# Performance work log

Measured on AMD Instinct MI355X. Metric: run time of the kernel, lower is better.

The kernel has to match this reference:

```python
import jax, jax.numpy as jnp
import numpy as np

N_NODES = 8192
N_EDGES = 65536
IN_DIM = 768
HIDDEN = 4096
N_CLASSES = 16


def setup_inputs() -> dict:
    key = jax.random.key(0)
    k1, k2, k3, k4 = jax.random.split(key, 4)
    x = jax.random.normal(k1, (N_NODES, IN_DIM), dtype=jnp.float32)
    edge_index = jax.random.randint(k2, (2, N_EDGES), 0, N_NODES, dtype=jnp.int64)
    # Glorot-ish init scale
    W1 = jax.random.normal(k3, (IN_DIM, HIDDEN), dtype=jnp.float32) * (1.0 / np.sqrt(IN_DIM))
    b1 = jnp.zeros((HIDDEN,), dtype=jnp.float32)
    W2 = jax.random.normal(k4, (HIDDEN, N_CLASSES), dtype=jnp.float32) * (1.0 / np.sqrt(HIDDEN))
    b2 = jnp.zeros((N_CLASSES,), dtype=jnp.float32)
    return {"x": x, "edge_index": edge_index, "W1": W1, "b1": b1, "W2": W2, "b2": b2}


def reference(x, edge_index, W1, b1, W2, b2):
    # GCNConv (PyG defaults): add self-loops, symmetric deg^-1/2 normalization,
    # transform-then-aggregate, plus bias. Then ReLU -> (dropout=identity at
    # inference) -> Linear -> log_softmax.
    N = x.shape[0]
    loops = jnp.arange(N, dtype=edge_index.dtype)
    src = jnp.concatenate([edge_index[0], loops])  # [E+N]
    dst = jnp.concatenate([edge_index[1], loops])  # [E+N]

    h = x @ W1  # [N, HIDDEN] dense GEMM

    deg = jax.ops.segment_sum(jnp.ones_like(dst, dtype=h.dtype), dst, num_segments=N)
    dinv = jnp.where(deg > 0, jax.lax.rsqrt(jnp.maximum(deg, 1e-12)), 0.0)
    norm = dinv[src] * dinv[dst]  # [E+N]

    agg = jax.ops.segment_sum(h[src] * norm[:, None], dst, num_segments=N)  # [N, HIDDEN]
    h = jax.nn.relu(agg + b1)

    logits = h @ W2 + b2  # [N, N_CLASSES]
    return jax.nn.log_softmax(logits, axis=1)
```

## Files before the change

### kernel.cpp

```cpp
#include <hip/hip_runtime.h>

#define N_NODES   8192
#define N_EDGES   65536
#define IN_DIM    768
#define HIDDEN    4096
#define N_CLASSES 16
#define SLOTS     64
#define NSLAB     16

typedef unsigned short ushort_t;
typedef __attribute__((ext_vector_type(8))) short bf16x8;
typedef __attribute__((ext_vector_type(4))) float f32x4;

__device__ __forceinline__ ushort_t f2bf(float f) {
    union { float f; unsigned i; } v; v.f = f;
    unsigned r = v.i + 0x7FFFu + ((v.i >> 16) & 1u);
    return (ushort_t)(r >> 16);
}
__device__ __forceinline__ float bf2f(ushort_t u) {
    union { unsigned i; float f; } v; v.i = ((unsigned)u) << 16; return v.f;
}

#define GLD_LDS16(gp, lp) \
    __builtin_amdgcn_global_load_lds((const __attribute__((address_space(1))) void*)(gp), \
                                     (__attribute__((address_space(3))) void*)(lp), 16, 0, 0)

__device__ __forceinline__ int esrc(const int* ei, int f32mode, int e) {
    return f32mode ? ei[e] : ei[2 * e];
}
__device__ __forceinline__ int edst(const int* ei, int f32mode, int e) {
    return f32mode ? ei[N_EDGES + e] : ei[2 * N_EDGES + 2 * e];
}

__global__ __launch_bounds__(256) void phase1(const float* __restrict__ x,
                                              ushort_t* __restrict__ xbf,
                                              const float* __restrict__ W2,
                                              ushort_t* __restrict__ W2T,
                                              const int* __restrict__ ei,
                                              int* __restrict__ cnt,
                                              int* __restrict__ slots,
                                              int* __restrict__ flag) {
    int b = blockIdx.x, t = threadIdx.x;
    if (b < 16) {
        __shared__ ushort_t ld[16 * 257];
        int k0 = b * 256;
        const float4* src = (const float4*)(W2 + (long)(k0 + t) * N_CLASSES);
        #pragma unroll
        for (int j = 0; j < 4; j++) {
            float4 v = src[j];
            ld[(j * 4 + 0) * 257 + t] = f2bf(v.x);
            ld[(j * 4 + 1) * 257 + t] = f2bf(v.y);
            ld[(j * 4 + 2) * 257 + t] = f2bf(v.z);
            ld[(j * 4 + 3) * 257 + t] = f2bf(v.w);
        }
        __syncthreads();
        #pragma unroll
        for (int c = 0; c < 16; c++)
            W2T[c * HIDDEN + k0 + t] = ld[c * 257 + t];
    } else if (b < 1552) {
        long i = (long)(b - 16) * 1024 + t;
        #pragma unroll
        for (int p = 0; p < 4; p++) {
            float4 v = ((const float4*)x)[i + p * 256];
            ushort4 r = { f2bf(v.x), f2bf(v.y), f2bf(v.z), f2bf(v.w) };
            ((ushort4*)xbf)[i + p * 256] = r;
        }
    } else {
        __shared__ int sv[256];
        int v = 0;
        for (int e = t; e < 4096; e += 256) v |= ei[2 * e + 1];
        sv[t] = v;
        __syncthreads();
        for (int off = 128; off > 0; off >>= 1) {
            if (t < off) sv[t] |= sv[t + off];
            __syncthreads();
        }
        int f = (sv[0] != 0) ? 1 : 0;
        if (b == 1552 && t == 0) *flag = f;
        int e = (b - 1552) * 256 + t;
        int s = esrc(ei, f, e), d = edst(ei, f, e);
        int p = atomicAdd(&cnt[d], 1);
        if (p < SLOTS) slots[d * SLOTS + p] = s;
    }
}

__global__ __launch_bounds__(256) void phase2(const float* __restrict__ W1,
                                              ushort_t* __restrict__ W1T,
                                              const ushort_t* __restrict__ xbf,
                                              const int* __restrict__ cnt,
                                              const int* __restrict__ slots,
                                              const int* __restrict__ ei,
                                              const int* __restrict__ flag,
                                              ushort_t* __restrict__ xagg) {
    int b = blockIdx.x, t = threadIdx.x;
    if (b < 3072) {
        __shared__ ushort_t tile[32][33];
        int n0 = (b & 127) * 32, k0 = (b >> 7) * 32;
        int tx = t & 31, ty = t >> 5;
        #pragma unroll
        for (int j = 0; j < 4; j++) {
            int k = ty * 4 + j;
            tile[k][tx] = f2bf(W1[(k0 + k) * HIDDEN + n0 + tx]);
        }
        __syncthreads();
        #pragma unroll
        for (int j = 0; j < 4; j++) {
            int n = ty * 4 + j;
            W1T[(n0 + n) * IN_DIM + k0 + tx] = tile[tx][n];
        }
        return;
    }
    if (t >= 192) return;
    int w = t >> 6, l = t & 63;
    int d = b - 3072;
    int fo = w * 256 + l * 4;
    int cd = cnt[d];
    float wd = rsqrtf((float)(cd + 1));
    ushort4 sv = *(const ushort4*)(xbf + (long)d * IN_DIM + fo);
    float a0 = wd * bf2f(sv.x), a1 = wd * bf2f(sv.y);
    float a2 = wd * bf2f(sv.z), a3 = wd * bf2f(sv.w);

    if (cd <= SLOTS) {
        const int* sl = slots + d * SLOTS;
        int j = 0;
        for (; j + 4 <= cd; j += 4) {
            int s0 = sl[j], s1 = sl[j + 1], s2 = sl[j + 2], s3 = sl[j + 3];
            float w0 = rsqrtf((float)(cnt[s0] + 1));
            float w1 = rsqrtf((float)(cnt[s1] + 1));
            float w2 = rsqrtf((float)(cnt[s2] + 1));
            float w3 = rsqrtf((float)(cnt[s3] + 1));
            ushort4 v0 = *(const ushort4*)(xbf + (long)s0 * IN_DIM + fo);
            ushort4 v1 = *(const ushort4*)(xbf + (long)s1 * IN_DIM + fo);
            ushort4 v2 = *(const ushort4*)(xbf + (long)s2 * IN_DIM + fo);
            ushort4 v3 = *(const ushort4*)(xbf + (long)s3 * IN_DIM + fo);
            a0 = fmaf(w0, bf2f(v0.x), a0); a1 = fmaf(w0, bf2f(v0.y), a1);
            a2 = fmaf(w0, bf2f(v0.z), a2); a3 = fmaf(w0, bf2f(v0.w), a3);
            a0 = fmaf(w1, bf2f(v1.x), a0); a1 = fmaf(w1, bf2f(v1.y), a1);
            a2 = fmaf(w1, bf2f(v1.z), a2); a3 = fmaf(w1, bf2f(v1.w), a3);
            a0 = fmaf(w2, bf2f(v2.x), a0); a1 = fmaf(w2, bf2f(v2.y), a1);
            a2 = fmaf(w2, bf2f(v2.z), a2); a3 = fmaf(w2, bf2f(v2.w), a3);
            a0 = fmaf(w3, bf2f(v3.x), a0); a1 = fmaf(w3, bf2f(v3.y), a1);
            a2 = fmaf(w3, bf2f(v3.z), a2); a3 = fmaf(w3, bf2f(v3.w), a3);
        }
        for (; j < cd; j++) {
            int s = sl[j];
            float ws = rsqrtf((float)(cnt[s] + 1));
            ushort4 v = *(const ushort4*)(xbf + (long)s * IN_DIM + fo);
            a0 = fmaf(ws, bf2f(v.x), a0); a1 = fmaf(ws, bf2f(v.y), a1);
            a2 = fmaf(ws, bf2f(v.z), a2); a3 = fmaf(ws, bf2f(v.w), a3);
        }
    } else {
        int f = *flag;
        for (int e = 0; e < N_EDGES; e++) {
            if (edst(ei, f, e) == d) {
                int s = esrc(ei, f, e);
                float ws = rsqrtf((float)(cnt[s] + 1));
                ushort4 v = *(const ushort4*)(xbf + (long)s * IN_DIM + fo);
                a0 = fmaf(ws, bf2f(v.x), a0); a1 = fmaf(ws, bf2f(v.y), a1);
                a2 = fmaf(ws, bf2f(v.z), a2); a3 = fmaf(ws, bf2f(v.w), a3);
            }
        }
    }
    ushort4 r = { f2bf(a0 * wd), f2bf(a1 * wd), f2bf(a2 * wd), f2bf(a3 * wd) };
    *(ushort4*)(xagg + (long)d * IN_DIM + fo) = r;
}

#define FENCE() asm volatile("" ::: "memory")
#define BAR()  do { FENCE(); __builtin_amdgcn_s_barrier(); FENCE(); } while (0)
#define VMCNT(n) asm volatile("s_waitcnt vmcnt(" #n ")" ::: "memory")
#define LGKM0()  asm volatile("s_waitcnt lgkmcnt(0)" ::: "memory")
#define PRIO(x)  __builtin_amdgcn_s_setprio(x)

__global__ __launch_bounds__(512, 2) void gemm1_fused(const ushort_t* __restrict__ A,
                                                      const ushort_t* __restrict__ Bt,
                                                      const float* __restrict__ b1,
                                                      const ushort_t* __restrict__ W2T,
                                                      float* __restrict__ part) {
    __shared__ ushort_t lds[65536];
    ushort_t* ldsA = lds;
    ushort_t* ldsB = lds + 32768;

    int t = threadIdx.x;
    int w = t >> 6, l = t & 63;
    int wm = w & 3, wn = w >> 2;
    int q = l >> 4, lm = l & 15;
    int bx = blockIdx.x & 15, by = blockIdx.x >> 4;
    int m0 = by * 256, n0 = bx * 256;

    int srow = t >> 3;
    int sg = (t & 7) ^ (srow & 7);
    const ushort_t* aS = A  + (long)(m0 + srow) * IN_DIM + sg * 8;
    const ushort_t* bS = Bt + (long)(n0 + srow) * IN_DIM + sg * 8;

#define STAGE_A(B_, h, ko) do { \
    GLD_LDS16(aS + (h) * 128 * IN_DIM + (ko),              ldsA + (B_) * 16384 + (h) * 8192 + w * 512); \
    GLD_LDS16(aS + ((h) * 128 + 64) * IN_DIM + (ko),       ldsA + (B_) * 16384 + (h) * 8192 + 4096 + w * 512); \
} while (0)
#define STAGE_B(B_, h, ko) do { \
    GLD_LDS16(bS + (h) * 128 * IN_DIM + (ko),              ldsB + (B_) * 16384 + (h) * 8192 + w * 512); \
    GLD_LDS16(bS + ((h) * 128 + 64) * IN_DIM + (ko),       ldsB + (B_) * 16384 + (h) * 8192 + 4096 + w * 512); \
} while (0)
#define LDA(dst, qm, B_) do { \
    const ushort_t* p_ = ldsA + (B_) * 16384 + (wm * 64 + (qm) * 32 + lm) * 64; \
    int x0_ = ((q) ^ (lm & 7)) * 8, x1_ = ((4 + q) ^ (lm & 7)) * 8; \
    dst[0][0] = *(const bf16x8*)(p_ + x0_);        dst[0][1] = *(const bf16x8*)(p_ + x1_); \
    dst[1][0] = *(const bf16x8*)(p_ + 1024 + x0_); dst[1][1] = *(const bf16x8*)(p_ + 1024 + x1_); \
} while (0)
#define LDB(dst, qn, B_) do { \
    const ushort_t* p_ = ldsB + (B_) * 16384 + (wn * 128 + (qn) * 64 + lm) * 64; \
    int x0_ = ((q) ^ (lm & 7)) * 8, x1_ = ((4 + q) ^ (lm & 7)) * 8; \
    dst[0][0] = *(const bf16x8*)(p_ + x0_);        dst[0][1] = *(const bf16x8*)(p_ + x1_); \
    dst[1][0] = *(const bf16x8*)(p_ + 1024 + x0_); dst[1][1] = *(const bf16x8*)(p_ + 1024 + x1_); \
    dst[2][0] = *(const bf16x8*)(p_ + 2048 + x0_); dst[2][1] = *(const bf16x8*)(p_ + 2048 + x1_); \
    dst[3][0] = *(const bf16x8*)(p_ + 3072 + x0_); dst[3][1] = *(const bf16x8*)(p_ + 3072 + x1_); \
} while (0)
#define MFMAQ(qm, qn, a_, b_) do { \
    _Pragma("unroll") for (int j_ = 0; j_ < 2; j_++) \
    _Pragma("unroll") for (int nt_ = 0; nt_ < 4; nt_++) \
    _Pragma("unroll") for (int mt_ = 0; mt_ < 2; mt_++) \
        acc[(qm) * 2 + mt_][(qn) * 4 + nt_] = __builtin_amdgcn_mfma_f32_16x16x32_bf16( \
            a_[mt_][j_], b_[nt_][j_], acc[(qm) * 2 + mt_][(qn) * 4 + nt_], 0, 0, 0); \
} while (0)

    int kA = 0, kB = 0;
    STAGE_A(0, 0, kA); STAGE_A(0, 1, kA); kA += 64;
    STAGE_B(0, 0, kB); STAGE_B(0, 1, kB); kB += 64;
    STAGE_A(1, 0, kA); STAGE_A(1, 1, kA); kA += 64;

    bf16x8 aq0[2][2], aq1[2][2], bq0[4][2], bq1[4][2];
    f32x4 acc[4][8] = {};

    VMCNT(4);
    BAR();

    #pragma unroll 1
    for (int it = 0; it < 5; ++it) {
        LDA(aq0, 0, 0); LDB(bq0, 0, 0); STAGE_B(1, 0, kB);
        BAR(); LGKM0(); PRIO(1); MFMAQ(0, 0, aq0, bq0); PRIO(0); BAR();
        LDA(aq1, 1, 0); STAGE_B(1, 1, kB); kB += 64;
        BAR(); LGKM0(); PRIO(1); MFMAQ(1, 0, aq1, bq0); PRIO(0); BAR();
        LDB(bq1, 1, 0); STAGE_A(0, 0, kA);
        BAR(); LGKM0(); PRIO(1); MFMAQ(1, 1, aq1, bq1); PRIO(0); BAR();
        STAGE_A(0, 1, kA); kA += 64;
        VMCNT(4);
        BAR(); PRIO(1); MFMAQ(0, 1, aq0, bq1); PRIO(0); BAR();
        LDA(aq0, 0, 1); LDB(bq0, 0, 1); STAGE_B(0, 0, kB);
        BAR(); LGKM0(); PRIO(1); MFMAQ(0, 0, aq0, bq0); PRIO(0); BAR();
        LDA(aq1, 1, 1); STAGE_B(0, 1, kB); kB += 64;
        BAR(); LGKM0(); PRIO(1); MFMAQ(1, 0, aq1, bq0); PRIO(0); BAR();
        LDB(bq1, 1, 1); STAGE_A(1, 0, kA);
        BAR(); LGKM0(); PRIO(1); MFMAQ(1, 1, aq1, bq1); PRIO(0); BAR();
        STAGE_A(1, 1, kA); kA += 64;
        VMCNT(4);
        BAR(); PRIO(1); MFMAQ(0, 1, aq0, bq1); PRIO(0); BAR();
    }
    LDA(aq0, 0, 0); LDB(bq0, 0, 0); STAGE_B(1, 0, kB);
    BAR(); LGKM0(); PRIO(1); MFMAQ(0, 0, aq0, bq0); PRIO(0); BAR();
    LDA(aq1, 1, 0); STAGE_B(1, 1, kB);
    BAR(); LGKM0(); PRIO(1); MFMAQ(1, 0, aq1, bq0); PRIO(0); BAR();
    LDB(bq1, 1, 0);
    BAR(); LGKM0(); PRIO(1); MFMAQ(1, 1, aq1, bq1); PRIO(0); BAR();
    VMCNT(0);
    BAR(); PRIO(1); MFMAQ(0, 1, aq0, bq1); PRIO(0); BAR();
    LDA(aq0, 0, 1); LDB(bq0, 0, 1);
    BAR(); LGKM0(); PRIO(1); MFMAQ(0, 0, aq0, bq0); PRIO(0); BAR();
    LDA(aq1, 1, 1);
    BAR(); LGKM0(); PRIO(1); MFMAQ(1, 0, aq1, bq0); PRIO(0); BAR();
    LDB(bq1, 1, 1);
    BAR(); LGKM0(); PRIO(1); MFMAQ(1, 1, aq1, bq1); PRIO(0); BAR();
    PRIO(1); MFMAQ(0, 1, aq0, bq1); PRIO(0);

    float bias[8];
    #pragma unroll
    for (int ng = 0; ng < 8; ng++) bias[ng] = b1[n0 + wn * 128 + ng * 16 + lm];
    bf16x8 w2f[2][2];
    #pragma unroll
    for (int eh = 0; eh < 2; eh++)
        #pragma unroll
        for (int kk = 0; kk < 2; kk++)
            w2f[eh][kk] = *(const bf16x8*)(W2T + (long)lm * HIDDEN + n0 + wn * 128 + eh * 64 + kk * 32 + q * 8);

    __syncthreads();
    ushort_t* slab = lds + w * 4096;
    f32x4 acc2[4] = {};
    #pragma unroll
    for (int eh = 0; eh < 2; eh++) {
        #pragma unroll
        for (int mg = 0; mg < 4; mg++)
            #pragma unroll
            for (int nt = 0; nt < 4; nt++) {
                int gc = nt * 2 + (lm >> 3);
                #pragma unroll
                for (int rr = 0; rr < 4; rr++) {
                    int row = mg * 16 + q * 4 + rr;
                    float v = acc[mg][eh * 4 + nt][rr] + bias[eh * 4 + nt];
                    v = v > 0.0f ? v : 0.0f;
                    slab[row * 64 + ((gc ^ (row & 7)) * 8) + (lm & 7)] = f2bf(v);
                }
            }
        #pragma unroll
        for (int kk = 0; kk < 2; kk++)
            #pragma unroll
            for (int mt2 = 0; mt2 < 4; mt2++) {
                bf16x8 a2 = *(const bf16x8*)(slab + (mt2 * 16 + lm) * 64 + (((kk * 4 + q) ^ (lm & 7)) * 8));
                acc2[mt2] = __builtin_amdgcn_mfma_f32_16x16x32_bf16(a2, w2f[eh][kk], acc2[mt2], 0, 0, 0);
            }
    }

    __syncthreads();
    float* psum = (float*)lds;
    if (wn == 1) {
        #pragma unroll
        for (int mt2 = 0; mt2 < 4; mt2++)
            #pragma unroll
            for (int rr = 0; rr < 4; rr++)
                psum[(wm * 64 + mt2 * 16 + q * 4 + rr) * 17 + lm] = acc2[mt2][rr];
    }
    __syncthreads();
    if (wn == 0) {
        float* pslab = part + ((long)bx * N_NODES + m0 + wm * 64) * N_CLASSES;
        #pragma unroll
        for (int mt2 = 0; mt2 < 4; mt2++)
            #pragma unroll
            for (int rr = 0; rr < 4; rr++) {
                int row = mt2 * 16 + q * 4 + rr;
                pslab[row * N_CLASSES + lm] = acc2[mt2][rr] + psum[(wm * 64 + row) * 17 + lm];
            }
    }
#undef STAGE_A
#undef STAGE_B
#undef LDA
#undef LDB
#undef MFMAQ
}

__global__ __launch_bounds__(256) void reduce_softmax(const float* __restrict__ part,
                                                      const float* __restrict__ b2,
                                                      float* __restrict__ out) {
    int t = threadIdx.x;
    int row = blockIdx.x * 16 + (t >> 4);
    int cls = t & 15;
    float v = b2[cls];
    #pragma unroll
    for (int s = 0; s < NSLAB; s++)
        v += part[((long)s * N_NODES + row) * N_CLASSES + cls];
    float mx = v;
    #pragma unroll
    for (int off = 1; off < 16; off <<= 1)
        mx = fmaxf(mx, __shfl_xor(mx, off, 64));
    float e = __expf(v - mx);
    float sm = e;
    #pragma unroll
    for (int off = 1; off < 16; off <<= 1)
        sm += __shfl_xor(sm, off, 64);
    out[(long)row * N_CLASSES + cls] = v - mx - __logf(sm);
}


extern "C" void kernel_launch(void* const* d_in, const int* in_sizes, int n_in,
                              void* d_out, int out_size, void* d_ws, size_t ws_size,
                              hipStream_t stream) {
    const float* x  = (const float*)d_in[0];
    const int*   ei = (const int*)d_in[1];
    const float* W1 = (const float*)d_in[2];
    const float* b1 = (const float*)d_in[3];
    const float* W2 = (const float*)d_in[4];
    const float* b2 = (const float*)d_in[5];
    float* out = (float*)d_out;
    char* ws = (char*)d_ws;

    float*    part  = (float*)(ws);
    ushort_t* xagg  = (ushort_t*)(ws + 16777216);
    ushort_t* xbf   = (ushort_t*)(ws + 29360128);
    ushort_t* W1T   = (ushort_t*)(ws + 41943040);
    ushort_t* W2T   = (ushort_t*)(ws + 48234496);
    int*      cnt   = (int*)(ws + 48365568);
    int*      slots = (int*)(ws + 48398336);
    int*      flag  = (int*)(ws + 50495488);

    hipMemsetAsync(cnt, 0, 32768, stream);
    phase1<<<1808, 256, 0, stream>>>(x, xbf, W2, W2T, ei, cnt, slots, flag);
    phase2<<<11264, 256, 0, stream>>>(W1, W1T, xbf, cnt, slots, ei, flag, xagg);
    gemm1_fused<<<(N_NODES / 256) * (HIDDEN / 256), 512, 0, stream>>>(xagg, W1T, b1, W2T, part);
    reduce_softmax<<<N_NODES / 16, 256, 0, stream>>>(part, b2, out);
}
```

Measured before the change: 159.7 us.

## Persistent two-tile GEMM with A reuse, move W1 transpose, repack aggregation

The fused GEMM now launches 256 blocks. Each block processes two consecutive 256-wide N tiles for one 256-row M tile and prefetches the next tile's A and B into free LDS buffers during the epilogue. The W1 transpose moves from phase2 into phase1, so the aggregation kernel only aggregates. That kernel now assigns one wavefront per node covering all 768 features, instead of three wavefronts per node with 64 idle threads per block. The aim is to cut block launch and tail overhead and to overlap the epilogue with the next tile's loads, at the cost of less GEMM parallelism (256 blocks) and more register pressure in the gather.

```diff
diff --git a/kernel.cpp b/kernel.cpp
--- a/kernel.cpp
+++ b/kernel.cpp
@@ -34,6 +34,8 @@
 
 __global__ __launch_bounds__(256) void phase1(const float* __restrict__ x,
                                               ushort_t* __restrict__ xbf,
+                                              const float* __restrict__ W1,
+                                              ushort_t* __restrict__ W1T,
                                               const float* __restrict__ W2,
                                               ushort_t* __restrict__ W2T,
                                               const int* __restrict__ ei,
@@ -65,7 +67,7 @@
             ushort4 r = { f2bf(v.x), f2bf(v.y), f2bf(v.z), f2bf(v.w) };
             ((ushort4*)xbf)[i + p * 256] = r;
         }
-    } else {
+    } else if (b < 1808) {
         __shared__ int sv[256];
         int v = 0;
         for (int e = t; e < 4096; e += 256) v |= ei[2 * e + 1];
@@ -81,45 +83,59 @@
         int s = esrc(ei, f, e), d = edst(ei, f, e);
         int p = atomicAdd(&cnt[d], 1);
         if (p < SLOTS) slots[d * SLOTS + p] = s;
+    } else {
+        __shared__ ushort_t tile[32][33];
+        int bt = b - 1808;
+        int n0 = (bt & 127) * 32, k0 = (bt >> 7) * 32;
+        int tx = t & 31, ty = t >> 5;
+        #pragma unroll
+        for (int j = 0; j < 4; j++) {
+            int k = ty * 4 + j;
+            tile[k][tx] = f2bf(W1[(k0 + k) * HIDDEN + n0 + tx]);
+        }
+        __syncthreads();
+        #pragma unroll
+        for (int j = 0; j < 4; j++) {
+            int n = ty * 4 + j;
+            W1T[(n0 + n) * IN_DIM + k0 + tx] = tile[tx][n];
+        }
     }
 }
 
-__global__ __launch_bounds__(256) void phase2(const float* __restrict__ W1,
-                                              ushort_t* __restrict__ W1T,
-                                              const ushort_t* __restrict__ xbf,
+#define ACC3(W_, v0_, v1_, v2_) do { \
+    a[0] = fmaf(W_, bf2f(v0_.x), a[0]); a[1]  = fmaf(W_, bf2f(v0_.y), a[1]); \
+    a[2] = fmaf(W_, bf2f(v0_.z), a[2]); a[3]  = fmaf(W_, bf2f(v0_.w), a[3]); \
+    a[4] = fmaf(W_, bf2f(v1_.x), a[4]); a[5]  = fmaf(W_, bf2f(v1_.y), a[5]); \
+    a[6] = fmaf(W_, bf2f(v1_.z), a[6]); a[7]  = fmaf(W_, bf2f(v1_.w), a[7]); \
+    a[8] = fmaf(W_, bf2f(v2_.x), a[8]); a[9]  = fmaf(W_, bf2f(v2_.y), a[9]); \
+    a[10] = fmaf(W_, bf2f(v2_.z), a[10]); a[11] = fmaf(W_, bf2f(v2_.w), a[11]); \
+} while (0)
+
+__global__ __launch_bounds__(256) void phase2(const ushort_t* __restrict__ xbf,
                                               const int* __restrict__ cnt,
                                               const int* __restrict__ slots,
                                               const int* __restrict__ ei,
                                               const int* __restrict__ flag,
                                               ushort_t* __restrict__ xagg) {
-    int b = blockIdx.x, t = threadIdx.x;
-    if (b < 3072) {
-        __shared__ ushort_t tile[32][33];
-        int n0 = (b & 127) * 32, k0 = (b >> 7) * 32;
-        int tx = t & 31, ty = t >> 5;
-        #pragma unroll
-        for (int j = 0; j < 4; j++) {
-            int k = ty * 4 + j;
-            tile[k][tx] = f2bf(W1[(k0 + k) * HIDDEN + n0 + tx]);
-        }
-        __syncthreads();
-        #pragma unroll
-        for (int j = 0; j < 4; j++) {
-            int n = ty * 4 + j;
-            W1T[(n0 + n) * IN_DIM + k0 + tx] = tile[tx][n];
-        }
-        return;
-    }
-    if (t >= 192) return;
+    int t = threadIdx.x;
     int w = t >> 6, l = t & 63;
-    int d = b - 3072;
-    int fo = w * 256 + l * 4;
+    int d = blockIdx.x * 4 + w;
+    int fo = l * 4;
     int cd = cnt[d];
     float wd = rsqrtf((float)(cd + 1));
-    ushort4 sv = *(const ushort4*)(xbf + (long)d * IN_DIM + fo);
-    float a0 = wd * bf2f(sv.x), a1 = wd * bf2f(sv.y);
-    float a2 = wd * bf2f(sv.z), a3 = wd * bf2f(sv.w);
-
+    float a[12];
+    {
+        const ushort_t* pr = xbf + (long)d * IN_DIM + fo;
+        ushort4 v0 = *(const ushort4*)(pr);
+        ushort4 v1 = *(const ushort4*)(pr + 256);
+        ushort4 v2 = *(const ushort4*)(pr + 512);
+        a[0] = wd * bf2f(v0.x); a[1]  = wd * bf2f(v0.y);
+        a[2] = wd * bf2f(v0.z); a[3]  = wd * bf2f(v0.w);
+        a[4] = wd * bf2f(v1.x); a[5]  = wd * bf2f(v1.y);
+        a[6] = wd * bf2f(v1.z); a[7]  = wd * bf2f(v1.w);
+        a[8] = wd * bf2f(v2.x); a[9]  = wd * bf2f(v2.y);
+        a[10] = wd * bf2f(v2.z); a[11] = wd * bf2f(v2.w);
+    }
     if (cd <= SLOTS) {
         const int* sl = slots + d * SLOTS;
         int j = 0;
@@ -129,25 +145,25 @@
             float w1 = rsqrtf((float)(cnt[s1] + 1));
             float w2 = rsqrtf((float)(cnt[s2] + 1));
             float w3 = rsqrtf((float)(cnt[s3] + 1));
-            ushort4 v0 = *(const ushort4*)(xbf + (long)s0 * IN_DIM + fo);
-            ushort4 v1 = *(const ushort4*)(xbf + (long)s1 * IN_DIM + fo);
-            ushort4 v2 = *(const ushort4*)(xbf + (long)s2 * IN_DIM + fo);
-            ushort4 v3 = *(const ushort4*)(xbf + (long)s3 * IN_DIM + fo);
-            a0 = fmaf(w0, bf2f(v0.x), a0); a1 = fmaf(w0, bf2f(v0.y), a1);
-            a2 = fmaf(w0, bf2f(v0.z), a2); a3 = fmaf(w0, bf2f(v0.w), a3);
-            a0 = fmaf(w1, bf2f(v1.x), a0); a1 = fmaf(w1, bf2f(v1.y), a1);
-            a2 = fmaf(w1, bf2f(v1.z), a2); a3 = fmaf(w1, bf2f(v1.w), a3);
-            a0 = fmaf(w2, bf2f(v2.x), a0); a1 = fmaf(w2, bf2f(v2.y), a1);
-            a2 = fmaf(w2, bf2f(v2.z), a2); a3 = fmaf(w2, bf2f(v2.w), a3);
-            a0 = fmaf(w3, bf2f(v3.x), a0); a1 = fmaf(w3, bf2f(v3.y), a1);
-            a2 = fmaf(w3, bf2f(v3.z), a2); a3 = fmaf(w3, bf2f(v3.w), a3);
+            const ushort_t* p0 = xbf + (long)s0 * IN_DIM + fo;
+            const ushort_t* p1 = xbf + (long)s1 * IN_DIM + fo;
+            const ushort_t* p2 = xbf + (long)s2 * IN_DIM + fo;
+            const ushort_t* p3 = xbf + (long)s3 * IN_DIM + fo;
+            ushort4 v00 = *(const ushort4*)(p0), v01 = *(const ushort4*)(p0 + 256), v02 = *(const ushort4*)(p0 + 512);
+            ushort4 v10 = *(const ushort4*)(p1), v11 = *(const ushort4*)(p1 + 256), v12 = *(const ushort4*)(p1 + 512);
+            ushort4 v20 = *(const ushort4*)(p2), v21 = *(const ushort4*)(p2 + 256), v22 = *(const ushort4*)(p2 + 512);
+            ushort4 v30 = *(const ushort4*)(p3), v31 = *(const ushort4*)(p3 + 256), v32 = *(const ushort4*)(p3 + 512);
+            ACC3(w0, v00, v01, v02);
+            ACC3(w1, v10, v11, v12);
+            ACC3(w2, v20, v21, v22);
+            ACC3(w3, v30, v31, v32);
         }
         for (; j < cd; j++) {
             int s = sl[j];
             float ws = rsqrtf((float)(cnt[s] + 1));
-            ushort4 v = *(const ushort4*)(xbf + (long)s * IN_DIM + fo);
-            a0 = fmaf(ws, bf2f(v.x), a0); a1 = fmaf(ws, bf2f(v.y), a1);
-            a2 = fmaf(ws, bf2f(v.z), a2); a3 = fmaf(ws, bf2f(v.w), a3);
+            const ushort_t* pp = xbf + (long)s * IN_DIM + fo;
+            ushort4 u0 = *(const ushort4*)(pp), u1 = *(const ushort4*)(pp + 256), u2 = *(const ushort4*)(pp + 512);
+            ACC3(ws, u0, u1, u2);
         }
     } else {
         int f = *flag;
@@ -155,14 +171,19 @@
             if (edst(ei, f, e) == d) {
                 int s = esrc(ei, f, e);
                 float ws = rsqrtf((float)(cnt[s] + 1));
-                ushort4 v = *(const ushort4*)(xbf + (long)s * IN_DIM + fo);
-                a0 = fmaf(ws, bf2f(v.x), a0); a1 = fmaf(ws, bf2f(v.y), a1);
-                a2 = fmaf(ws, bf2f(v.z), a2); a3 = fmaf(ws, bf2f(v.w), a3);
+                const ushort_t* pp = xbf + (long)s * IN_DIM + fo;
+                ushort4 u0 = *(const ushort4*)(pp), u1 = *(const ushort4*)(pp + 256), u2 = *(const ushort4*)(pp + 512);
+                ACC3(ws, u0, u1, u2);
             }
         }
     }
-    ushort4 r = { f2bf(a0 * wd), f2bf(a1 * wd), f2bf(a2 * wd), f2bf(a3 * wd) };
-    *(ushort4*)(xagg + (long)d * IN_DIM + fo) = r;
+    ushort_t* po = xagg + (long)d * IN_DIM + fo;
+    ushort4 r0 = { f2bf(a[0] * wd), f2bf(a[1] * wd), f2bf(a[2] * wd), f2bf(a[3] * wd) };
+    ushort4 r1 = { f2bf(a[4] * wd), f2bf(a[5] * wd), f2bf(a[6] * wd), f2bf(a[7] * wd) };
+    ushort4 r2 = { f2bf(a[8] * wd), f2bf(a[9] * wd), f2bf(a[10] * wd), f2bf(a[11] * wd) };
+    *(ushort4*)(po) = r0;
+    *(ushort4*)(po + 256) = r1;
+    *(ushort4*)(po + 512) = r2;
 }
 
 #define FENCE() asm volatile("" ::: "memory")
@@ -184,21 +205,21 @@
     int w = t >> 6, l = t & 63;
     int wm = w & 3, wn = w >> 2;
     int q = l >> 4, lm = l & 15;
-    int bx = blockIdx.x & 15, by = blockIdx.x >> 4;
-    int m0 = by * 256, n0 = bx * 256;
+    int p8 = blockIdx.x & 7, by = blockIdx.x >> 3;
+    int m0 = by * 256;
 
     int srow = t >> 3;
     int sg = (t & 7) ^ (srow & 7);
-    const ushort_t* aS = A  + (long)(m0 + srow) * IN_DIM + sg * 8;
-    const ushort_t* bS = Bt + (long)(n0 + srow) * IN_DIM + sg * 8;
+    const ushort_t* aS = A + (long)(m0 + srow) * IN_DIM + sg * 8;
+    const ushort_t* bS = Bt + (long)(p8 * 512 + srow) * IN_DIM + sg * 8;
 
 #define STAGE_A(B_, h, ko) do { \
-    GLD_LDS16(aS + (h) * 128 * IN_DIM + (ko),              ldsA + (B_) * 16384 + (h) * 8192 + w * 512); \
-    GLD_LDS16(aS + ((h) * 128 + 64) * IN_DIM + (ko),       ldsA + (B_) * 16384 + (h) * 8192 + 4096 + w * 512); \
-} while (0)
-#define STAGE_B(B_, h, ko) do { \
-    GLD_LDS16(bS + (h) * 128 * IN_DIM + (ko),              ldsB + (B_) * 16384 + (h) * 8192 + w * 512); \
-    GLD_LDS16(bS + ((h) * 128 + 64) * IN_DIM + (ko),       ldsB + (B_) * 16384 + (h) * 8192 + 4096 + w * 512); \
+    GLD_LDS16(aS + (h) * 128 * IN_DIM + (ko),            ldsA + (B_) * 16384 + (h) * 8192 + w * 512); \
+    GLD_LDS16(aS + ((h) * 128 + 64) * IN_DIM + (ko),     ldsA + (B_) * 16384 + (h) * 8192 + 4096 + w * 512); \
+} while (0)
+#define STAGE_B(bp, B_, h, ko) do { \
+    GLD_LDS16((bp) + (h) * 128 * IN_DIM + (ko),          ldsB + (B_) * 16384 + (h) * 8192 + w * 512); \
+    GLD_LDS16((bp) + ((h) * 128 + 64) * IN_DIM + (ko),   ldsB + (B_) * 16384 + (h) * 8192 + 4096 + w * 512); \
 } while (0)
 #define LDA(dst, qm, B_) do { \
     const ushort_t* p_ = ldsA + (B_) * 16384 + (wm * 64 + (qm) * 32 + lm) * 64; \
@@ -222,110 +243,124 @@
             a_[mt_][j_], b_[nt_][j_], acc[(qm) * 2 + mt_][(qn) * 4 + nt_], 0, 0, 0); \
 } while (0)
 
-    int kA = 0, kB = 0;
-    STAGE_A(0, 0, kA); STAGE_A(0, 1, kA); kA += 64;
-    STAGE_B(0, 0, kB); STAGE_B(0, 1, kB); kB += 64;
-    STAGE_A(1, 0, kA); STAGE_A(1, 1, kA); kA += 64;
+    STAGE_A(0, 0, 0); STAGE_A(0, 1, 0);
+    STAGE_B(bS, 0, 0, 0); STAGE_B(bS, 0, 1, 0);
+    STAGE_A(1, 0, 64); STAGE_A(1, 1, 64);
 
     bf16x8 aq0[2][2], aq1[2][2], bq0[4][2], bq1[4][2];
-    f32x4 acc[4][8] = {};
-
-    VMCNT(4);
-    BAR();
 
     #pragma unroll 1
-    for (int it = 0; it < 5; ++it) {
-        LDA(aq0, 0, 0); LDB(bq0, 0, 0); STAGE_B(1, 0, kB);
+    for (int tile = 0; tile < 2; ++tile) {
+        int n0 = p8 * 512 + tile * 256;
+        f32x4 acc[4][8] = {};
+        int kA = 128, kB = 64;
+
+        VMCNT(4);
+        BAR();
+
+        #pragma unroll 1
+        for (int it = 0; it < 5; ++it) {
+            LDA(aq0, 0, 0); LDB(bq0, 0, 0); STAGE_B(bS, 1, 0, kB);
+            BAR(); LGKM0(); PRIO(1); MFMAQ(0, 0, aq0, bq0); PRIO(0); BAR();
+            LDA(aq1, 1, 0); STAGE_B(bS, 1, 1, kB); kB += 64;
+            BAR(); LGKM0(); PRIO(1); MFMAQ(1, 0, aq1, bq0); PRIO(0); BAR();
+            LDB(bq1, 1, 0); STAGE_A(0, 0, kA);
+            BAR(); LGKM0(); PRIO(1); MFMAQ(1, 1, aq1, bq1); PRIO(0); BAR();
+            STAGE_A(0, 1, kA); kA += 64;
+            VMCNT(4);
+            BAR(); PRIO(1); MFMAQ(0, 1, aq0, bq1); PRIO(0); BAR();
+            LDA(aq0, 0, 1); LDB(bq0, 0, 1); STAGE_B(bS, 0, 0, kB);
+            BAR(); LGKM0(); PRIO(1); MFMAQ(0, 0, aq0, bq0); PRIO(0); BAR();
+            LDA(aq1, 1, 1); STAGE_B(bS, 0, 1, kB); kB += 64;
+            BAR(); LGKM0(); PRIO(1); MFMAQ(1, 0, aq1, bq0); PRIO(0); BAR();
+            LDB(bq1, 1, 1); STAGE_A(1, 0, kA);
+            BAR(); LGKM0(); PRIO(1); MFMAQ(1, 1, aq1, bq1); PRIO(0); BAR();
+            STAGE_A(1, 1, kA); kA += 64;
+            VMCNT(4);
+            BAR(); PRIO(1); MFMAQ(0, 1, aq0, bq1); PRIO(0); BAR();
+        }
+        LDA(aq0, 0, 0); LDB(bq0, 0, 0); STAGE_B(bS, 1, 0, kB);
         BAR(); LGKM0(); PRIO(1); MFMAQ(0, 0, aq0, bq0); PRIO(0); BAR();
-        LDA(aq1, 1, 0); STAGE_B(1, 1, kB); kB += 64;
+        LDA(aq1, 1, 0); STAGE_B(bS, 1, 1, kB);
         BAR(); LGKM0(); PRIO(1); MFMAQ(1, 0, aq1, bq0); PRIO(0); BAR();
-        LDB(bq1, 1, 0); STAGE_A(0, 0, kA);
+        LDB(bq1, 1, 0);
         BAR(); LGKM0(); PRIO(1); MFMAQ(1, 1, aq1, bq1); PRIO(0); BAR();
-        STAGE_A(0, 1, kA); kA += 64;
-        VMCNT(4);
+        VMCNT(0);
         BAR(); PRIO(1); MFMAQ(0, 1, aq0, bq1); PRIO(0); BAR();
-        LDA(aq0, 0, 1); LDB(bq0, 0, 1); STAGE_B(0, 0, kB);
+        LDA(aq0, 0, 1); LDB(bq0, 0, 1);
         BAR(); LGKM0(); PRIO(1); MFMAQ(0, 0, aq0, bq0); PRIO(0); BAR();
-        LDA(aq1, 1, 1); STAGE_B(0, 1, kB); kB += 64;
+        LDA(aq1, 1, 1);
         BAR(); LGKM0(); PRIO(1); MFMAQ(1, 0, aq1, bq0); PRIO(0); BAR();
-        LDB(bq1, 1, 1); STAGE_A(1, 0, kA);
+        LDB(bq1, 1, 1);
         BAR(); LGKM0(); PRIO(1); MFMAQ(1, 1, aq1, bq1); PRIO(0); BAR();
-        STAGE_A(1, 1, kA); kA += 64;
-        VMCNT(4);
-        BAR(); PRIO(1); MFMAQ(0, 1, aq0, bq1); PRIO(0); BAR();
-    }
-    LDA(aq0, 0, 0); LDB(bq0, 0, 0); STAGE_B(1, 0, kB);
-    BAR(); LGKM0(); PRIO(1); MFMAQ(0, 0, aq0, bq0); PRIO(0); BAR();
-    LDA(aq1, 1, 0); STAGE_B(1, 1, kB);
-    BAR(); LGKM0(); PRIO(1); MFMAQ(1, 0, aq1, bq0); PRIO(0); BAR();
-    LDB(bq1, 1, 0);
-    BAR(); LGKM0(); PRIO(1); MFMAQ(1, 1, aq1, bq1); PRIO(0); BAR();
-    VMCNT(0);
-    BAR(); PRIO(1); MFMAQ(0, 1, aq0, bq1); PRIO(0); BAR();
-    LDA(aq0, 0, 1); LDB(bq0, 0, 1);
-    BAR(); LGKM0(); PRIO(1); MFMAQ(0, 0, aq0, bq0); PRIO(0); BAR();
-    LDA(aq1, 1, 1);
-    BAR(); LGKM0(); PRIO(1); MFMAQ(1, 0, aq1, bq0); PRIO(0); BAR();
-    LDB(bq1, 1, 1);
-    BAR(); LGKM0(); PRIO(1); MFMAQ(1, 1, aq1, bq1); PRIO(0); BAR();
-    PRIO(1); MFMAQ(0, 1, aq0, bq1); PRIO(0);
-
-    float bias[8];
-    #pragma unroll
-    for (int ng = 0; ng < 8; ng++) bias[ng] = b1[n0 + wn * 128 + ng * 16 + lm];
-    bf16x8 w2f[2][2];
-    #pragma unroll
-    for (int eh = 0; eh < 2; eh++)
-        #pragma unroll
-        for (int kk = 0; kk < 2; kk++)
-            w2f[eh][kk] = *(const bf16x8*)(W2T + (long)lm * HIDDEN + n0 + wn * 128 + eh * 64 + kk * 32 + q * 8);
-
-    __syncthreads();
-    ushort_t* slab = lds + w * 4096;
-    f32x4 acc2[4] = {};
-    #pragma unroll
-    for (int eh = 0; eh < 2; eh++) {
-        #pragma unroll
-        for (int mg = 0; mg < 4; mg++)
+        PRIO(1); MFMAQ(0, 1, aq0, bq1); PRIO(0);
+
+        float bias[8];
+        #pragma unroll
+        for (int ng = 0; ng < 8; ng++) bias[ng] = b1[n0 + wn * 128 + ng * 16 + lm];
+        bf16x8 w2f[2][2];
+        #pragma unroll
+        for (int eh = 0; eh < 2; eh++)
             #pragma unroll
-            for (int nt = 0; nt < 4; nt++) {
-                int gc = nt * 2 + (lm >> 3);
+            for (int kk = 0; kk < 2; kk++)
+                w2f[eh][kk] = *(const bf16x8*)(W2T + (long)lm * HIDDEN + n0 + wn * 128 + eh * 64 + kk * 32 + q * 8);
+
+        BAR();
+        if (tile == 0) {
+            STAGE_A(0, 0, 0); STAGE_A(0, 1, 0);
+            STAGE_B(bS + 256 * IN_DIM, 0, 0, 0); STAGE_B(bS + 256 * IN_DIM, 0, 1, 0);
+        }
+        ushort_t* slab = (w < 4) ? (ldsA + 16384 + w * 4096)
+                                 : (ldsB + 16384 + (w - 4) * 4096);
+        f32x4 acc2[4] = {};
+        #pragma unroll
+        for (int eh = 0; eh < 2; eh++) {
+            #pragma unroll
+            for (int mg = 0; mg < 4; mg++)
+                #pragma unroll
+                for (int nt = 0; nt < 4; nt++) {
+                    int gc = nt * 2 + (lm >> 3);
+                    #pragma unroll
+                    for (int rr = 0; rr < 4; rr++) {
+                        int row = mg * 16 + q * 4 + rr;
+                        float v = acc[mg][eh * 4 + nt][rr] + bias[eh * 4 + nt];
+                        v = v > 0.0f ? v : 0.0f;
+                        slab[row * 64 + ((gc ^ (row & 7)) * 8) + (lm & 7)] = f2bf(v);
+                    }
+                }
+            #pragma unroll
+            for (int kk = 0; kk < 2; kk++)
+                #pragma unroll
+                for (int mt2 = 0; mt2 < 4; mt2++) {
+                    bf16x8 a2 = *(const bf16x8*)(slab + (mt2 * 16 + lm) * 64 + (((kk * 4 + q) ^ (lm & 7)) * 8));
+                    acc2[mt2] = __builtin_amdgcn_mfma_f32_16x16x32_bf16(a2, w2f[eh][kk], acc2[mt2], 0, 0, 0);
+                }
+        }
+
+        BAR();
+        if (tile == 0) { STAGE_A(1, 0, 64); STAGE_A(1, 1, 64); }
+        float* psum = (float*)(ldsB + 16384);
+        if (wn == 1) {
+            #pragma unroll
+            for (int mt2 = 0; mt2 < 4; mt2++)
+                #pragma unroll
+                for (int rr = 0; rr < 4; rr++)
+                    psum[(wm * 64 + mt2 * 16 + q * 4 + rr) * 17 + lm] = acc2[mt2][rr];
+        }
+        LGKM0();
+        BAR();
+        if (wn == 0) {
+            int bx = p8 * 2 + tile;
+            float* pslab = part + ((long)bx * N_NODES + m0 + wm * 64) * N_CLASSES;
+            #pragma unroll
+            for (int mt2 = 0; mt2 < 4; mt2++)
                 #pragma unroll
                 for (int rr = 0; rr < 4; rr++) {
-                    int row = mg * 16 + q * 4 + rr;
-                    float v = acc[mg][eh * 4 + nt][rr] + bias[eh * 4 + nt];
-                    v = v > 0.0f ? v : 0.0f;
-                    slab[row * 64 + ((gc ^ (row & 7)) * 8) + (lm & 7)] = f2bf(v);
+                    int row = mt2 * 16 + q * 4 + rr;
+                    pslab[row * N_CLASSES + lm] = acc2[mt2][rr] + psum[(wm * 64 + row) * 17 + lm];
                 }
-            }
-        #pragma unroll
-        for (int kk = 0; kk < 2; kk++)
-            #pragma unroll
-            for (int mt2 = 0; mt2 < 4; mt2++) {
-                bf16x8 a2 = *(const bf16x8*)(slab + (mt2 * 16 + lm) * 64 + (((kk * 4 + q) ^ (lm & 7)) * 8));
-                acc2[mt2] = __builtin_amdgcn_mfma_f32_16x16x32_bf16(a2, w2f[eh][kk], acc2[mt2], 0, 0, 0);
-            }
-    }
-
-    __syncthreads();
-    float* psum = (float*)lds;
-    if (wn == 1) {
-        #pragma unroll
-        for (int mt2 = 0; mt2 < 4; mt2++)
-            #pragma unroll
-            for (int rr = 0; rr < 4; rr++)
-                psum[(wm * 64 + mt2 * 16 + q * 4 + rr) * 17 + lm] = acc2[mt2][rr];
-    }
-    __syncthreads();
-    if (wn == 0) {
-        float* pslab = part + ((long)bx * N_NODES + m0 + wm * 64) * N_CLASSES;
-        #pragma unroll
-        for (int mt2 = 0; mt2 < 4; mt2++)
-            #pragma unroll
-            for (int rr = 0; rr < 4; rr++) {
-                int row = mt2 * 16 + q * 4 + rr;
-                pslab[row * N_CLASSES + lm] = acc2[mt2][rr] + psum[(wm * 64 + row) * 17 + lm];
-            }
+        }
+        bS += 256 * IN_DIM;
     }
 #undef STAGE_A
 #undef STAGE_B
@@ -379,8 +414,8 @@
     int*      flag  = (int*)(ws + 50495488);
 
     hipMemsetAsync(cnt, 0, 32768, stream);
-    phase1<<<1808, 256, 0, stream>>>(x, xbf, W2, W2T, ei, cnt, slots, flag);
-    phase2<<<11264, 256, 0, stream>>>(W1, W1T, xbf, cnt, slots, ei, flag, xagg);
-    gemm1_fused<<<(N_NODES / 256) * (HIDDEN / 256), 512, 0, stream>>>(xagg, W1T, b1, W2T, part);
+    phase1<<<4880, 256, 0, stream>>>(x, xbf, W1, W1T, W2, W2T, ei, cnt, slots, flag);
+    phase2<<<2048, 256, 0, stream>>>(xbf, cnt, slots, ei, flag, xagg);
+    gemm1_fused<<<256, 512, 0, stream>>>(xagg, W1T, b1, W2T, part);
     reduce_softmax<<<N_NODES / 16, 256, 0, stream>>>(part, b2, out);
 }
```

Measured after the change: 207.0 us. 1.3x slower.
